# Performance work log

Hardware: AMD Instinct MI355X
Metric: run time of the kernel (lower is better)

The kernel has to match this reference:

```python
import jax, jax.numpy as jnp
import numpy as np
from jax import lax

EPS = 1e-5
DN = ('NCHW', 'OIHW', 'NCHW')


def setup_inputs() -> dict:
    key = jax.random.key(0)
    ks = jax.random.split(key, 16)
    B = 8192
    # uniform(0,1): every pixel nonzero => all voxels active => sparse conv == dense conv
    x = jax.random.uniform(ks[0], (B, 1, 28, 28), dtype=jnp.float32)

    def conv_params(kw, kb, c_in, c_out, k):
        scale = 1.0 / np.sqrt(c_in * k * k)
        w = jax.random.normal(kw, (c_out, c_in, k, k), dtype=jnp.float32) * scale
        b = jax.random.normal(kb, (c_out,), dtype=jnp.float32) * scale
        return w, b

    w0, b0 = conv_params(ks[1], ks[2], 1, 32, 3)
    w1, b1 = conv_params(ks[3], ks[4], 32, 64, 2)
    w2, b2 = conv_params(ks[5], ks[6], 64, 128, 2)
    # BatchNorm affine params (init: gamma=1, beta=0)
    g0, be0 = jnp.ones((32,), jnp.float32), jnp.zeros((32,), jnp.float32)
    g1, be1 = jnp.ones((64,), jnp.float32), jnp.zeros((64,), jnp.float32)
    g2, be2 = jnp.ones((128,), jnp.float32), jnp.zeros((128,), jnp.float32)
    w_fc = jax.random.normal(ks[7], (10, 128), dtype=jnp.float32) * (1.0 / np.sqrt(128))
    b_fc = jax.random.normal(ks[8], (10,), dtype=jnp.float32) * (1.0 / np.sqrt(128))
    return dict(x=x, w0=w0, b0=b0, g0=g0, be0=be0,
                w1=w1, b1=b1, g1=g1, be1=be1,
                w2=w2, b2=b2, g2=g2, be2=be2,
                w_fc=w_fc, b_fc=b_fc)


def _conv_bn_relu(x, w, b, g, be, stride, padding):
    # sparse conv on fully-active grid == dense conv
    y = lax.conv_general_dilated(x, w, (stride, stride), padding,
                                 dimension_numbers=DN)
    y = y + b[None, :, None, None]
    # BatchNorm1d over (N_active, C) == stats over batch+spatial (biased var)
    mean = jnp.mean(y, axis=(0, 2, 3))
    var = jnp.var(y, axis=(0, 2, 3))
    y = (y - mean[None, :, None, None]) * lax.rsqrt(var + EPS)[None, :, None, None]
    y = y * g[None, :, None, None] + be[None, :, None, None]
    return jax.nn.relu(y)


def reference(x, w0, b0, g0, be0, w1, b1, g1, be1, w2, b2, g2, be2, w_fc, b_fc):
    h = _conv_bn_relu(x, w0, b0, g0, be0, 1, 'SAME')    # (B,32,28,28)
    h = _conv_bn_relu(h, w1, b1, g1, be1, 2, 'VALID')   # (B,64,14,14)
    h = _conv_bn_relu(h, w2, b2, g2, be2, 2, 'VALID')   # (B,128,7,7)
    pooled = jnp.mean(h, axis=(2, 3))                    # AdaptiveAvgPool2d(1)+Flatten
    return pooled @ w_fc.T + b_fc                        # (B, n_classes)
```

## Files before the change

kernel.cpp:

```cpp
#include <hip/hip_runtime.h>
#include <hip/hip_bf16.h>

typedef __bf16 bf16x8 __attribute__((ext_vector_type(8)));
typedef float  f32x4  __attribute__((ext_vector_type(4)));

#define BSZ 8192

__global__ __launch_bounds__(256) void k_stats0(const float* __restrict__ x,
                                                float* __restrict__ part0,
                                                const float* __restrict__ w1,
                                                const float* __restrict__ w2,
                                                __bf16* __restrict__ w1b,
                                                __bf16* __restrict__ w2b) {
    __shared__ float sred[4 * 54];
    const int tid = threadIdx.x;
    {
        int t = blockIdx.x * 256 + tid;
        if (t < 8192) {
            int oc = t >> 7, k = t & 127, c = k & 31, d = k >> 5;
            w1b[t] = (__bf16)w1[oc * 128 + c * 4 + d];
        }
        if (t < 32768) {
            int oc = t >> 8, k = t & 255, c = k & 63, d = k >> 6;
            w2b[t] = (__bf16)w2[oc * 256 + c * 4 + d];
        }
    }
    float a[54];
#pragma unroll
    for (int i = 0; i < 54; i++) a[i] = 0.f;
    const int total = BSZ * 784;
    for (int p = blockIdx.x * 256 + tid; p < total; p += gridDim.x * 256) {
        int b = p / 784, pix = p - b * 784;
        int y = pix / 28, xx = pix - y * 28;
        const float* xb = x + (long)b * 784;
        float nv[9];
#pragma unroll
        for (int dy = 0; dy < 3; dy++) {
            int yy = y + dy - 1;
#pragma unroll
            for (int dx = 0; dx < 3; dx++) {
                int x2 = xx + dx - 1;
                nv[dy * 3 + dx] = (yy >= 0 && yy < 28 && x2 >= 0 && x2 < 28) ? xb[yy * 28 + x2] : 0.f;
            }
        }
        int idx = 0;
#pragma unroll
        for (int t2 = 0; t2 < 9; t2++) {
            float vt = nv[t2];
            a[45 + t2] += vt;
#pragma unroll
            for (int u = t2; u < 9; u++) { a[idx] += vt * nv[u]; idx++; }
        }
    }
#pragma unroll
    for (int i = 0; i < 54; i++) {
        float v = a[i];
        v += __shfl_xor(v, 1);  v += __shfl_xor(v, 2);  v += __shfl_xor(v, 4);
        v += __shfl_xor(v, 8);  v += __shfl_xor(v, 16); v += __shfl_xor(v, 32);
        a[i] = v;
    }
    const int l = tid & 63, w = tid >> 6;
    if (l == 0) {
#pragma unroll
        for (int i = 0; i < 54; i++) sred[w * 54 + i] = a[i];
    }
    __syncthreads();
    if (tid < 54)
        part0[blockIdx.x * 64 + tid] = sred[tid] + sred[54 + tid] + sred[108 + tid] + sred[162 + tid];
}

__global__ void k_fin0(const float* __restrict__ part0, const float* __restrict__ w0,
                       const float* __restrict__ g0, const float* __restrict__ be0,
                       float* __restrict__ abc0) {
    __shared__ float red[4 * 54];
    int t = threadIdx.x, c = t & 63, g = t >> 6;
    if (c < 54) {
        float acc = 0.f;
        for (int i = g; i < 1024; i += 4) acc += part0[i * 64 + c];
        red[g * 54 + c] = acc;
    }
    __syncthreads();
    if (t < 54) red[t] = red[t] + red[54 + t] + red[108 + t] + red[162 + t];
    __syncthreads();
    if (t < 32) {
        float wv[9];
#pragma unroll
        for (int tap = 0; tap < 9; tap++) wv[tap] = w0[t * 9 + tap];
        float sum = 0.f, sq = 0.f;
        int idx = 0;
#pragma unroll
        for (int ta = 0; ta < 9; ta++) {
            sum = fmaf(wv[ta], red[45 + ta], sum);
#pragma unroll
            for (int u = ta; u < 9; u++) {
                float coef = (u == ta) ? 1.f : 2.f;
                sq = fmaf(coef * wv[ta] * wv[u], red[idx], sq);
                idx++;
            }
        }
        float cnt = (float)BSZ * 784.f;
        float mean = sum / cnt;
        float var = sq / cnt - mean * mean;
        float A = g0[t] * rsqrtf(var + 1e-5f);
#pragma unroll
        for (int tap = 0; tap < 9; tap++)
            abc0[(t >> 3) * 72 + tap * 8 + (t & 7)] = A * wv[tap];
        abc0[288 + t] = be0[t] - mean * A;
    }
}

__global__ __launch_bounds__(256) void k_conv01(const float* __restrict__ x,
                                                const float* __restrict__ abc0,
                                                const __bf16* __restrict__ w1b,
                                                __bf16* __restrict__ h1,
                                                float* __restrict__ part1) {
    __shared__ float xs[30 * 30];
    __shared__ __attribute__((aligned(16))) __bf16 sAt[2][16 * 136];
    const int tid = threadIdx.x;
    if (tid < 116) {
        int idx;
        if (tid < 30)      idx = tid;
        else if (tid < 60) idx = 29 * 30 + (tid - 30);
        else if (tid < 88) idx = (tid - 60 + 1) * 30;
        else               idx = (tid - 88 + 1) * 30 + 29;
        xs[idx] = 0.f;
    }
    const int pgu = __builtin_amdgcn_readfirstlane(tid >> 6);
    const float* wfp = abc0 + pgu * 72;
    float wf[72];
#pragma unroll
    for (int i = 0; i < 72; i++) wf[i] = wfp[i];
    float c0r[8];
#pragma unroll
    for (int j = 0; j < 8; j++) c0r[j] = abc0[288 + pgu * 8 + j];

    const int pi = tid & 15, pd = (tid >> 4) & 3;
    const int w = tid >> 6, l = tid & 63, q = l >> 4, n = l & 15;
    const int oc = w * 16 + n;
    bf16x8 fbv[4];
#pragma unroll
    for (int kc = 0; kc < 4; kc++)
        fbv[kc] = *(const bf16x8*)&w1b[oc * 128 + kc * 32 + q * 8];

    for (int img = 0; img < 4; img++) {
        const int b = blockIdx.x * 4 + img;
        for (int j = tid; j < 784; j += 256) {
            int yy = j / 28, xx2 = j - yy * 28;
            xs[(yy + 1) * 30 + xx2 + 1] = x[(long)b * 784 + j];
        }
        __syncthreads();
        float ssum = 0.f, ssq = 0.f;
        __bf16* hb = h1 + (long)b * 12544 + (q * 4) * 64 + oc;
        for (int mt = 0; mt < 13; mt++) {
            __bf16* dst = &sAt[mt & 1][pi * 136 + pd * 32 + pgu * 8];
            int m = mt * 16 + pi;
            bf16x8 pk;
            if (m < 196) {
                int my = m / 14, mx = m - my * 14;
                int y0 = my * 2 + (pd >> 1), x0 = mx * 2 + (pd & 1);
                float nv[9];
#pragma unroll
                for (int dy = 0; dy < 3; dy++)
#pragma unroll
                    for (int dx = 0; dx < 3; dx++)
                        nv[dy * 3 + dx] = xs[(y0 + dy) * 30 + x0 + dx];
                float a[8];
#pragma unroll
                for (int j = 0; j < 8; j++) a[j] = c0r[j];
#pragma unroll
                for (int t = 0; t < 9; t++) {
                    float nvt = nv[t];
#pragma unroll
                    for (int j = 0; j < 8; j++) a[j] = fmaf(nvt, wf[t * 8 + j], a[j]);
                }
#pragma unroll
                for (int j = 0; j < 8; j++) pk[j] = (__bf16)fmaxf(a[j], 0.f);
            } else {
#pragma unroll
                for (int j = 0; j < 8; j++) pk[j] = (__bf16)0.0f;
            }
            *(bf16x8*)dst = pk;
            __syncthreads();
            const __bf16* sa = &sAt[mt & 1][n * 136 + q * 8];
            f32x4 acc = {0.f, 0.f, 0.f, 0.f};
#pragma unroll
            for (int kc = 0; kc < 4; kc++) {
                bf16x8 fav = *(const bf16x8*)&sa[kc * 32];
                acc = __builtin_amdgcn_mfma_f32_16x16x32_bf16(fav, fbv[kc], acc, 0, 0, 0);
            }
            bool valid = (mt < 12) | (q == 0);
            __bf16* hp = hb + mt * 16 * 64;
#pragma unroll
            for (int r = 0; r < 4; r++) {
                __bf16 hv = (__bf16)acc[r];
                if (valid) hp[r * 64] = hv;
                float fv = (float)hv;
                ssum += fv; ssq += fv * fv;
            }
        }
        ssum += __shfl_xor(ssum, 16); ssum += __shfl_xor(ssum, 32);
        ssq  += __shfl_xor(ssq, 16);  ssq  += __shfl_xor(ssq, 32);
        if (l < 16) {
            part1[(long)oc * BSZ + b] = ssum;
            part1[(long)(64 + oc) * BSZ + b] = ssq;
        }
    }
}

__global__ __launch_bounds__(256) void k_redfin(const float* __restrict__ part,
                                                const float* __restrict__ g,
                                                const float* __restrict__ be,
                                                float* __restrict__ abc,
                                                int C, float cnt) {
    __shared__ float s1[256], s2[256];
    const int c = blockIdx.x, tid = threadIdx.x;
    float a = 0.f, bq = 0.f;
    const float* p1 = part + (long)c * BSZ;
    const float* p2 = part + (long)(C + c) * BSZ;
    for (int i = tid; i < BSZ; i += 256) { a += p1[i]; bq += p2[i]; }
    s1[tid] = a; s2[tid] = bq;
    __syncthreads();
    for (int s = 128; s > 0; s >>= 1) {
        if (tid < s) { s1[tid] += s1[tid + s]; s2[tid] += s2[tid + s]; }
        __syncthreads();
    }
    if (tid == 0) {
        float mean = s1[0] / cnt;
        float var = s2[0] / cnt - mean * mean;
        float A = g[c] * rsqrtf(var + 1e-5f);
        abc[c] = A;
        abc[C + c] = be[c] - mean * A;
    }
}

__global__ __launch_bounds__(256) void k_conv2s(__bf16* __restrict__ h1,
                                                const __bf16* __restrict__ w2b,
                                                const float* __restrict__ abc1,
                                                float* __restrict__ part2) {
    __shared__ __attribute__((aligned(16))) __bf16 sAt[2][16 * 264];
    __shared__ __attribute__((aligned(16))) __bf16 zt[16 * 136];
    __shared__ float sbn1[128];
    const int tid = threadIdx.x;
    if (tid < 128) sbn1[tid] = abc1[tid];
    const int w = tid >> 6, l = tid & 63, q = l >> 4, n = l & 15;
    bf16x8 fbv[2][8];
#pragma unroll
    for (int ntl = 0; ntl < 2; ntl++) {
        int oc = (2 * w + ntl) * 16 + n;
#pragma unroll
        for (int kc = 0; kc < 8; kc++)
            fbv[ntl][kc] = *(const bf16x8*)&w2b[oc * 256 + kc * 32 + q * 8];
    }
    __syncthreads();

    for (int img = 0; img < 4; img++) {
        const int b = blockIdx.x * 4 + img;
        __bf16* src = h1 + (long)b * 12544;
        float ssum[2] = {0.f, 0.f}, ssq[2] = {0.f, 0.f};
        for (int mt = 0; mt < 4; mt++) {
#pragma unroll
            for (int it = 0; it < 2; it++) {
                int idx = it * 256 + tid;
                int rl = idx >> 5, o = (idx & 31) * 8;
                int r = mt * 16 + rl;
                bf16x8 wv;
                if (r < 49) {
                    int d = o >> 6, c = o & 63;
                    int py = r / 7, px = r - py * 7;
                    int msrc = (2 * py + (d >> 1)) * 14 + 2 * px + (d & 1);
                    bf16x8 v = *(const bf16x8*)&src[msrc * 64 + c];
#pragma unroll
                    for (int j = 0; j < 8; j++) {
                        float f = fmaxf((float)v[j] * sbn1[c + j] + sbn1[64 + c + j], 0.f);
                        wv[j] = (__bf16)f;
                    }
                } else {
#pragma unroll
                    for (int j = 0; j < 8; j++) wv[j] = (__bf16)0.0f;
                }
                *(bf16x8*)&sAt[mt & 1][rl * 264 + o] = wv;
            }
            __syncthreads();
            bf16x8 fav[8];
#pragma unroll
            for (int kc = 0; kc < 8; kc++)
                fav[kc] = *(const bf16x8*)&sAt[mt & 1][n * 264 + kc * 32 + q * 8];
#pragma unroll
            for (int ntl = 0; ntl < 2; ntl++) {
                f32x4 acc = {0.f, 0.f, 0.f, 0.f};
#pragma unroll
                for (int kc = 0; kc < 8; kc++)
                    acc = __builtin_amdgcn_mfma_f32_16x16x32_bf16(fav[kc], fbv[ntl][kc], acc, 0, 0, 0);
#pragma unroll
                for (int rr = 0; rr < 4; rr++) {
                    __bf16 hv = (__bf16)acc[rr];
                    zt[(q * 4 + rr) * 136 + (2 * w + ntl) * 16 + n] = hv;
                    float fv = (float)hv;
                    ssum[ntl] += fv; ssq[ntl] += fv * fv;
                }
            }
            __syncthreads();
            {
                int row = tid >> 4, o = (tid & 15) * 8;
                int m = mt * 16 + row;
                if (m < 49) {
                    bf16x8 zv = *(const bf16x8*)&zt[row * 136 + o];
                    *(bf16x8*)&src[m * 128 + o] = zv;
                }
            }
        }
#pragma unroll
        for (int ntl = 0; ntl < 2; ntl++) {
            ssum[ntl] += __shfl_xor(ssum[ntl], 16); ssum[ntl] += __shfl_xor(ssum[ntl], 32);
            ssq[ntl]  += __shfl_xor(ssq[ntl], 16);  ssq[ntl]  += __shfl_xor(ssq[ntl], 32);
        }
        if (l < 16) {
#pragma unroll
            for (int ntl = 0; ntl < 2; ntl++) {
                int oc = (2 * w + ntl) * 16 + l;
                part2[(long)oc * BSZ + b] = ssum[ntl];
                part2[(long)(128 + oc) * BSZ + b] = ssq[ntl];
            }
        }
    }
}

__global__ __launch_bounds__(256) void k_final(const __bf16* __restrict__ z2,
                                               const float* __restrict__ abc2,
                                               const float* __restrict__ wfc,
                                               const float* __restrict__ bfc,
                                               float* __restrict__ out) {
    __shared__ float sbn2[256];
    __shared__ float pp[16 * 128];
    __shared__ float pooled[128];
    __shared__ float fcred[80];
    const int tid = threadIdx.x;
    sbn2[tid] = abc2[tid];
    __syncthreads();
    const int g = tid & 15, c0 = g * 8, rg = tid >> 4;
    for (int img = 0; img < 4; img++) {
        const int b = blockIdx.x * 4 + img;
        const __bf16* src = z2 + (long)b * 12544;
        float acc[8];
#pragma unroll
        for (int q = 0; q < 8; q++) acc[q] = 0.f;
        for (int rr = rg; rr < 49; rr += 16) {
            bf16x8 v = *(const bf16x8*)&src[rr * 128 + c0];
#pragma unroll
            for (int q = 0; q < 8; q++) {
                float f = fmaxf((float)v[q] * sbn2[c0 + q] + sbn2[128 + c0 + q], 0.f);
                acc[q] += f;
            }
        }
        *(f32x4*)&pp[rg * 128 + c0]     = *(f32x4*)&acc[0];
        *(f32x4*)&pp[rg * 128 + c0 + 4] = *(f32x4*)&acc[4];
        __syncthreads();
        if (tid < 128) {
            float s = 0.f;
#pragma unroll
            for (int r = 0; r < 16; r++) s += pp[r * 128 + tid];
            pooled[tid] = s * (1.f / 49.f);
        }
        __syncthreads();
        if (tid < 80) {
            int o = tid >> 3, s = tid & 7;
            float a = 0.f;
#pragma unroll
            for (int j = 0; j < 16; j++) a = fmaf(pooled[s * 16 + j], wfc[o * 128 + s * 16 + j], a);
            fcred[tid] = a;
        }
        __syncthreads();
        if (tid < 10) {
            float a = bfc[tid];
#pragma unroll
            for (int s = 0; s < 8; s++) a += fcred[tid * 8 + s];
            out[(long)b * 10 + tid] = a;
        }
    }
}

extern "C" void kernel_launch(void* const* d_in, const int* in_sizes, int n_in,
                              void* d_out, int out_size, void* d_ws, size_t ws_size,
                              hipStream_t stream) {
    const float* x   = (const float*)d_in[0];
    const float* w0  = (const float*)d_in[1];
    const float* g0  = (const float*)d_in[3];
    const float* be0 = (const float*)d_in[4];
    const float* w1  = (const float*)d_in[5];
    const float* g1  = (const float*)d_in[7];
    const float* be1 = (const float*)d_in[8];
    const float* w2  = (const float*)d_in[9];
    const float* g2  = (const float*)d_in[11];
    const float* be2 = (const float*)d_in[12];
    const float* wfc = (const float*)d_in[13];
    const float* bfc = (const float*)d_in[14];
    float* out = (float*)d_out;

    float* ws    = (float*)d_ws;
    float* part0 = ws;
    float* abc0  = part0 + 1024 * 64;
    float* part1 = abc0 + 320;
    float* abc1  = part1 + 128 * BSZ;
    float* part2 = abc1 + 128;
    float* abc2  = part2 + 256 * BSZ;
    __bf16* w1b  = (__bf16*)(abc2 + 256);
    __bf16* w2b  = w1b + 8192;
    __bf16* h1   = w2b + 32768;

    k_stats0<<<dim3(1024), dim3(256), 0, stream>>>(x, part0, w1, w2, w1b, w2b);
    k_fin0<<<dim3(1), dim3(256), 0, stream>>>(part0, w0, g0, be0, abc0);
    k_conv01<<<dim3(BSZ / 4), dim3(256), 0, stream>>>(x, abc0, w1b, h1, part1);
    k_redfin<<<dim3(64), dim3(256), 0, stream>>>(part1, g1, be1, abc1, 64, (float)(BSZ * 196));
    k_conv2s<<<dim3(BSZ / 4), dim3(256), 0, stream>>>(h1, w2b, abc1, part2);
    k_redfin<<<dim3(128), dim3(256), 0, stream>>>(part2, g2, be2, abc2, 128, (float)(BSZ * 49));
    k_final<<<dim3(BSZ / 4), dim3(256), 0, stream>>>(h1, abc2, wfc, bfc, out);
}
```

Before: 411.6 us.

## Compute first conv on MFMA using split bf16 hi/lo operands

The 3x3 first-layer conv plus BN plus ReLU moves from per-thread scalar FMAs over fp32 registers to MFMA bf16 instructions. Input pixels are stored in shared memory as packed hi/lo bf16 pairs, and the BN-folded weights are likewise split into main and correction parts. This keeps near-fp32 accuracy while using the matrix cores. The stats grid is also shrunk to 1008 blocks, and the freed part0 space is reused for the new weight table. This relies on the hidden stats kernel still covering all inputs at the smaller grid, and it adds packing overhead for each image load.

```diff
diff --git a/kernel.cpp b/kernel.cpp
--- a/kernel.cpp
+++ b/kernel.cpp
@@ -5,6 +5,9 @@
 typedef float  f32x4  __attribute__((ext_vector_type(4)));
 
 #define BSZ 8192
+
+union BW2 { __bf16 b[2]; unsigned int u; };
+union FR  { unsigned int u[4]; bf16x8 v; };
 
 __global__ __launch_bounds__(256) void k_stats0(const float* __restrict__ x,
                                                 float* __restrict__ part0,
@@ -71,12 +74,12 @@
 
 __global__ void k_fin0(const float* __restrict__ part0, const float* __restrict__ w0,
                        const float* __restrict__ g0, const float* __restrict__ be0,
-                       float* __restrict__ abc0) {
+                       float* __restrict__ abc0, __bf16* __restrict__ wcv) {
     __shared__ float red[4 * 54];
     int t = threadIdx.x, c = t & 63, g = t >> 6;
     if (c < 54) {
         float acc = 0.f;
-        for (int i = g; i < 1024; i += 4) acc += part0[i * 64 + c];
+        for (int i = g; i < 1008; i += 4) acc += part0[i * 64 + c];
         red[g * 54 + c] = acc;
     }
     __syncthreads();
@@ -102,84 +105,95 @@
         float mean = sum / cnt;
         float var = sq / cnt - mean * mean;
         float A = g0[t] * rsqrtf(var + 1e-5f);
-#pragma unroll
-        for (int tap = 0; tap < 9; tap++)
-            abc0[(t >> 3) * 72 + tap * 8 + (t & 7)] = A * wv[tap];
         abc0[288 + t] = be0[t] - mean * A;
-    }
-}
-
-__global__ __launch_bounds__(256) void k_conv01(const float* __restrict__ x,
-                                                const float* __restrict__ abc0,
-                                                const __bf16* __restrict__ w1b,
-                                                __bf16* __restrict__ h1,
-                                                float* __restrict__ part1) {
-    __shared__ float xs[30 * 30];
+        int nn = t >> 1, hh = t & 1;
+#pragma unroll
+        for (int j = 0; j < 4; j++) {
+#pragma unroll
+            for (int e = 0; e < 8; e++) {
+                float vm = 0.f, vc = 0.f;
+                if (j < 3) {
+                    int i = e >> 1;
+                    if (i < 3) vm = A * wv[j * 3 + i];
+                    if (e < 3) {
+                        float wfull = A * wv[j * 3 + e];
+                        vc = wfull - (float)((__bf16)wfull);
+                    }
+                }
+                wcv[hh * 512 + j * 128 + nn * 8 + e]       = (__bf16)vm;
+                wcv[(2 + hh) * 512 + j * 128 + nn * 8 + e] = (__bf16)vc;
+            }
+        }
+    }
+}
+
+__global__ __launch_bounds__(256, 4) void k_conv01(const float* __restrict__ x,
+                                                   const float* __restrict__ abc0,
+                                                   const __bf16* __restrict__ wcv,
+                                                   const __bf16* __restrict__ w1b,
+                                                   __bf16* __restrict__ h1,
+                                                   float* __restrict__ part1) {
+    __shared__ unsigned int xs2[31 * 30];
     __shared__ __attribute__((aligned(16))) __bf16 sAt[2][16 * 136];
     const int tid = threadIdx.x;
-    if (tid < 116) {
-        int idx;
-        if (tid < 30)      idx = tid;
-        else if (tid < 60) idx = 29 * 30 + (tid - 30);
-        else if (tid < 88) idx = (tid - 60 + 1) * 30;
-        else               idx = (tid - 88 + 1) * 30 + 29;
-        xs[idx] = 0.f;
-    }
-    const int pgu = __builtin_amdgcn_readfirstlane(tid >> 6);
-    const float* wfp = abc0 + pgu * 72;
-    float wf[72];
-#pragma unroll
-    for (int i = 0; i < 72; i++) wf[i] = wfp[i];
-    float c0r[8];
-#pragma unroll
-    for (int j = 0; j < 8; j++) c0r[j] = abc0[288 + pgu * 8 + j];
-
-    const int pi = tid & 15, pd = (tid >> 4) & 3;
     const int w = tid >> 6, l = tid & 63, q = l >> 4, n = l & 15;
+    const int d1 = w >> 1, d0 = w & 1;
+    for (int i = tid; i < 930; i += 256) xs2[i] = 0u;
+    bf16x8 bw[2][2];
+#pragma unroll
+    for (int ps = 0; ps < 2; ps++)
+#pragma unroll
+        for (int h = 0; h < 2; h++)
+            bw[ps][h] = *(const bf16x8*)&wcv[(ps * 2 + h) * 512 + q * 128 + n * 8];
+    const float bias0 = abc0[288 + 2 * n];
+    const float bias1 = abc0[288 + 2 * n + 1];
     const int oc = w * 16 + n;
     bf16x8 fbv[4];
 #pragma unroll
     for (int kc = 0; kc < 4; kc++)
         fbv[kc] = *(const bf16x8*)&w1b[oc * 128 + kc * 32 + q * 8];
+    __syncthreads();
 
     for (int img = 0; img < 4; img++) {
         const int b = blockIdx.x * 4 + img;
-        for (int j = tid; j < 784; j += 256) {
-            int yy = j / 28, xx2 = j - yy * 28;
-            xs[(yy + 1) * 30 + xx2 + 1] = x[(long)b * 784 + j];
+        for (int jj = tid; jj < 784; jj += 256) {
+            int yy = jj / 28, xx2 = jj - yy * 28;
+            float f = x[(long)b * 784 + jj];
+            __bf16 hi = (__bf16)f;
+            __bf16 lo = (__bf16)(f - (float)hi);
+            BW2 pk; pk.b[0] = hi; pk.b[1] = lo;
+            xs2[(yy + 1) * 30 + xx2 + 1] = pk.u;
         }
         __syncthreads();
         float ssum = 0.f, ssq = 0.f;
         __bf16* hb = h1 + (long)b * 12544 + (q * 4) * 64 + oc;
         for (int mt = 0; mt < 13; mt++) {
-            __bf16* dst = &sAt[mt & 1][pi * 136 + pd * 32 + pgu * 8];
-            int m = mt * 16 + pi;
-            bf16x8 pk;
-            if (m < 196) {
-                int my = m / 14, mx = m - my * 14;
-                int y0 = my * 2 + (pd >> 1), x0 = mx * 2 + (pd & 1);
-                float nv[9];
-#pragma unroll
-                for (int dy = 0; dy < 3; dy++)
-#pragma unroll
-                    for (int dx = 0; dx < 3; dx++)
-                        nv[dy * 3 + dx] = xs[(y0 + dy) * 30 + x0 + dx];
-                float a[8];
-#pragma unroll
-                for (int j = 0; j < 8; j++) a[j] = c0r[j];
-#pragma unroll
-                for (int t = 0; t < 9; t++) {
-                    float nvt = nv[t];
-#pragma unroll
-                    for (int j = 0; j < 8; j++) a[j] = fmaf(nvt, wf[t * 8 + j], a[j]);
+            {
+                int m = mt * 16 + n;
+                int mv = m < 195 ? m : 195;
+                int my = mv / 14, mx = mv - my * 14;
+                int row = 2 * my + d1 + q, col = 2 * mx + d0;
+                const unsigned int* p = &xs2[row * 30 + col];
+                unsigned int u0 = p[0], u1 = p[1], u2 = p[2];
+                FR a0, a1;
+                a0.u[0] = u0; a0.u[1] = u1; a0.u[2] = u2; a0.u[3] = 0u;
+                a1.u[0] = (u0 & 0xffffu) | (u1 << 16); a1.u[1] = u2 & 0xffffu;
+                a1.u[2] = 0u; a1.u[3] = 0u;
+                f32x4 ac0 = {bias0, bias0, bias0, bias0};
+                f32x4 ac1 = {bias1, bias1, bias1, bias1};
+                ac0 = __builtin_amdgcn_mfma_f32_16x16x32_bf16(a0.v, bw[0][0], ac0, 0, 0, 0);
+                ac1 = __builtin_amdgcn_mfma_f32_16x16x32_bf16(a0.v, bw[0][1], ac1, 0, 0, 0);
+                ac0 = __builtin_amdgcn_mfma_f32_16x16x32_bf16(a1.v, bw[1][0], ac0, 0, 0, 0);
+                ac1 = __builtin_amdgcn_mfma_f32_16x16x32_bf16(a1.v, bw[1][1], ac1, 0, 0, 0);
+#pragma unroll
+                for (int r = 0; r < 4; r++) {
+                    int mrow = q * 4 + r;
+                    float v0 = fmaxf(ac0[r], 0.f), v1 = fmaxf(ac1[r], 0.f);
+                    if (mt * 16 + mrow >= 196) { v0 = 0.f; v1 = 0.f; }
+                    BW2 pk; pk.b[0] = (__bf16)v0; pk.b[1] = (__bf16)v1;
+                    *(unsigned int*)&sAt[mt & 1][mrow * 136 + w * 32 + 2 * n] = pk.u;
                 }
-#pragma unroll
-                for (int j = 0; j < 8; j++) pk[j] = (__bf16)fmaxf(a[j], 0.f);
-            } else {
-#pragma unroll
-                for (int j = 0; j < 8; j++) pk[j] = (__bf16)0.0f;
-            }
-            *(bf16x8*)dst = pk;
+            }
             __syncthreads();
             const __bf16* sa = &sAt[mt & 1][n * 136 + q * 8];
             f32x4 acc = {0.f, 0.f, 0.f, 0.f};
@@ -398,6 +412,7 @@
 
     float* ws    = (float*)d_ws;
     float* part0 = ws;
+    __bf16* wcv  = (__bf16*)(part0 + 1008 * 64);
     float* abc0  = part0 + 1024 * 64;
     float* part1 = abc0 + 320;
     float* abc1  = part1 + 128 * BSZ;
@@ -407,9 +422,9 @@
     __bf16* w2b  = w1b + 8192;
     __bf16* h1   = w2b + 32768;
 
-    k_stats0<<<dim3(1024), dim3(256), 0, stream>>>(x, part0, w1, w2, w1b, w2b);
-    k_fin0<<<dim3(1), dim3(256), 0, stream>>>(part0, w0, g0, be0, abc0);
-    k_conv01<<<dim3(BSZ / 4), dim3(256), 0, stream>>>(x, abc0, w1b, h1, part1);
+    k_stats0<<<dim3(1008), dim3(256), 0, stream>>>(x, part0, w1, w2, w1b, w2b);
+    k_fin0<<<dim3(1), dim3(256), 0, stream>>>(part0, w0, g0, be0, abc0, wcv);
+    k_conv01<<<dim3(BSZ / 4), dim3(256), 0, stream>>>(x, abc0, wcv, w1b, h1, part1);
     k_redfin<<<dim3(64), dim3(256), 0, stream>>>(part1, g1, be1, abc1, 64, (float)(BSZ * 196));
     k_conv2s<<<dim3(BSZ / 4), dim3(256), 0, stream>>>(h1, w2b, abc1, part2);
     k_redfin<<<dim3(128), dim3(256), 0, stream>>>(part2, g2, be2, abc2, 128, (float)(BSZ * 49));
```

Result: faster. 389.3 us (-5.4%).
